# Kernel tuning notes

Measured on AMD Instinct MI355X. Metric: run time of the kernel, lower is better.

The kernel has to match this reference:

```python
import jax, jax.numpy as jnp
import numpy as np
from jax import lax

D_MODEL = 128

def _pad_same(x, kh, kw):
    ph, pw = kh - 1, kw - 1
    return jnp.pad(x, ((0, 0), (0, 0), (ph // 2, ph - ph // 2), (pw // 2, pw - pw // 2)))

def _conv(x, w, b):
    y = lax.conv_general_dilated(x, w, (1, 1), 'VALID', dimension_numbers=('NCHW', 'OIHW', 'NCHW'))
    return y + b[None, :, None, None]

def _group_norm(x, g, b, groups, eps=1e-5):
    N, C, H, W = x.shape
    xr = x.reshape(N, groups, -1)
    m = xr.mean(axis=2, keepdims=True)
    v = xr.var(axis=2, keepdims=True)
    xn = ((xr - m) / jnp.sqrt(v + eps)).reshape(N, C, H, W)
    return xn * g[None, :, None, None] + b[None, :, None, None]

def _maxpool(x, kh, kw):
    return lax.reduce_window(x, -jnp.inf, lax.max, (1, 1, kh, kw), (1, 1, kh, kw), 'VALID')

def _l2norm(x, axis):
    # torch F.normalize(p=2): x / max(||x||, eps)
    return x / jnp.maximum(jnp.linalg.norm(x, axis=axis, keepdims=True), 1e-12)

def _pos_encoding(S, d):
    pos = jnp.arange(S, dtype=jnp.float32)[:, None]
    div = jnp.exp(jnp.arange(0, d, 2, dtype=jnp.float32) * (-float(np.log(10000.0)) / d))
    pe = jnp.zeros((S, d), dtype=jnp.float32)
    pe = pe.at[:, 0::2].set(jnp.sin(pos * div)).at[:, 1::2].set(jnp.cos(pos * div))
    return pe

def setup_inputs() -> dict:
    key = jax.random.key(0)
    ks = jax.random.split(key, 16)
    def w(k, shape, fan_in):
        return jax.random.normal(k, shape, dtype=jnp.float32) * (1.0 / np.sqrt(fan_in))
    return {
        'x': jax.random.normal(ks[0], (1, 1024, 72, 64), dtype=jnp.float32),
        'conv1_w': w(ks[1], (32, 1, 6, 4), 1 * 6 * 4),
        'conv1_b': jnp.zeros((32,), jnp.float32),
        'gn1_g': jnp.ones((32,), jnp.float32), 'gn1_b': jnp.zeros((32,), jnp.float32),
        'conv2_w': w(ks[2], (64, 32, 6, 4), 32 * 6 * 4),
        'conv2_b': jnp.zeros((64,), jnp.float32),
        'gn2_g': jnp.ones((64,), jnp.float32), 'gn2_b': jnp.zeros((64,), jnp.float32),
        'conv3_w': w(ks[3], (128, 64, 6, 4), 64 * 6 * 4),
        'conv3_b': jnp.zeros((128,), jnp.float32),
        'gn3_g': jnp.ones((128,), jnp.float32), 'gn3_b': jnp.zeros((128,), jnp.float32),
        'fc1_w': w(ks[4], (128, 1024), 1024),
        'fc1_b': jnp.zeros((128,), jnp.float32),
        'wq': w(ks[5], (128, 128), 128), 'bq': jnp.zeros((128,), jnp.float32),
        'wk': w(ks[6], (128, 128), 128), 'bk': jnp.zeros((128,), jnp.float32),
        'wv': w(ks[7], (128, 128), 128), 'bv': jnp.zeros((128,), jnp.float32),
    }

def reference(x, conv1_w, conv1_b, gn1_g, gn1_b, conv2_w, conv2_b, gn2_g, gn2_b,
              conv3_w, conv3_b, gn3_g, gn3_b, fc1_w, fc1_b, wq, bq, wk, bk, wv, bv):
    selu = jax.nn.selu
    # x: [1, S, 72, 64] -> transpose(0,1): [S, 1, 72, 64] (S frames, 1 channel)
    h = jnp.transpose(x, (1, 0, 2, 3))
    h = _maxpool(_group_norm(selu(_conv(_pad_same(h, 6, 4), conv1_w, conv1_b)), gn1_g, gn1_b, 32), 2, 4)
    h = _maxpool(_group_norm(selu(_conv(_pad_same(h, 6, 4), conv2_w, conv2_b)), gn2_g, gn2_b, 32), 3, 4)
    h = _maxpool(_group_norm(selu(_conv(_pad_same(h, 6, 4), conv3_w, conv3_b)), gn3_g, gn3_b, 32), 3, 2)
    e = h.reshape(h.shape[0], -1)                       # [S, 1024]
    e = _l2norm(selu(e @ fc1_w.T + fc1_b), axis=1)      # [S, 128]
    S = e.shape[0]
    q = selu(e @ wq.T + bq)
    k = selu(e @ wk.T + bk)
    v = selu(e @ wv.T + bv)
    k_pos = k + _pos_encoding(S, D_MODEL)               # PE added to K only
    attn = jax.nn.softmax((q @ k_pos.T) / jnp.sqrt(jnp.float32(D_MODEL)), axis=-1)  # [S, S]
    # torch F.normalize default dim=1 on [1,S,D] -> normalize over the sequence axis
    out = _l2norm(attn @ v, axis=0) + e
    ea = _l2norm(out, axis=0)                           # [S, 128]
    # pairwise L2 distances (self-similarity matrix), then 1 - d/max(d)
    sq = jnp.sum(ea * ea, axis=1)
    d2 = jnp.maximum(sq[:, None] + sq[None, :] - 2.0 * (ea @ ea.T), 0.0)
    d = jnp.sqrt(d2 + 1e-12)
    return 1.0 - d / jnp.max(d)
```

## Files before the change

kernel.cpp:

```cpp
#include <hip/hip_runtime.h>
#include <hip/hip_bf16.h>
#include <math.h>

#define SELU_SCALE 1.0507009873554805f
#define SELU_SA    1.7580993408473766f

typedef __attribute__((ext_vector_type(8))) short short8;
typedef __attribute__((ext_vector_type(4))) short short4v;
typedef __attribute__((ext_vector_type(4))) float f32x4;

__device__ __forceinline__ float selu_f(float x){
    return x > 0.f ? SELU_SCALE * x : fmaf(SELU_SA, __expf(x), -SELU_SA);
}

__device__ __forceinline__ unsigned short bfc(float v){
    __hip_bfloat16 h = __float2bfloat16(v);
    return __builtin_bit_cast(unsigned short, h);
}
__device__ __forceinline__ float f_bf(unsigned short u){
    unsigned int x = ((unsigned int)u) << 16;
    return __builtin_bit_cast(float, x);
}

__device__ __forceinline__ float warp_max(float v){
    #pragma unroll
    for(int o=32;o>0;o>>=1) v = fmaxf(v,__shfl_down(v,o,64));
    return v;
}

__global__ void k_prep(const float* __restrict__ f1w, const float* __restrict__ wq,
                       const float* __restrict__ wk, const float* __restrict__ wv,
                       const float* __restrict__ w1, const float* __restrict__ w2,
                       const float* __restrict__ w3,
                       float* __restrict__ wt, float* __restrict__ wqt,
                       float* __restrict__ wkt, float* __restrict__ wvt,
                       short* __restrict__ w1bf, short* __restrict__ w2bf,
                       short* __restrict__ w3bf){
    int idx = blockIdx.x*256 + threadIdx.x;
    if(idx < 131072){ int r = idx >> 10, cc = idx & 1023; wt[cc*128 + r] = f1w[idx]; return; }
    idx -= 131072;
    if(idx < 16384){ int r = idx >> 7, cc = idx & 127; wqt[cc*128 + r] = wq[idx]; return; }
    idx -= 16384;
    if(idx < 16384){ int r = idx >> 7, cc = idx & 127; wkt[cc*128 + r] = wk[idx]; return; }
    idx -= 16384;
    if(idx < 16384){ int r = idx >> 7, cc = idx & 127; wvt[cc*128 + r] = wv[idx]; return; }
    idx -= 16384;
    if(idx < 49152){
        int t = idx >> 11, rem = idx & 2047;
        int oc = rem >> 5, ic = rem & 31;
        w2bf[idx] = (short)bfc(w2[oc*768 + ic*24 + t]);
        return;
    }
    idx -= 49152;
    if(idx < 196608){
        int t = idx >> 13, rem = idx & 8191;
        int oc = rem >> 6, ic = rem & 63;
        w3bf[idx] = (short)bfc(w3[oc*1536 + ic*24 + t]);
        return;
    }
    idx -= 196608;
    if(idx < 1024){
        int oc = idx >> 5, k = idx & 31;
        w1bf[idx] = (k < 24) ? (short)bfc(w1[oc*24 + k]) : (short)0;
    }
}

__global__ __launch_bounds__(768,1) void k_conv1m(
    const float* __restrict__ x, const short* __restrict__ w1bf,
    const float* __restrict__ bias, const float* __restrict__ g,
    const float* __restrict__ be, float* __restrict__ out)
{
    int s = blockIdx.x, tid = threadIdx.x;
    int l = tid & 63, wv = tid >> 6;
    int c = l & 15, qr = l >> 4;
    __shared__ char smem[127728];
    short* sdup = (short*)smem;
    char* pmaxb = smem + 41712;
    char* pminb = smem + 83184;
    float* sredf = (float*)(smem + 124656);
    __shared__ float scsh[64];

    const float* xs = x + (size_t)s*4608;
    for(int i = tid; i < 5056; i += 768){
        int yp = i >> 6, xx = i & 63;
        unsigned long long pk = 0ull;
        if(yp >= 2 && yp < 74){
            const float* row = xs + (yp-2)*64;
            #pragma unroll
            for(int t=0;t<4;t++){
                int cp = xx + t;
                float f = (cp>=1 && cp<65) ? row[cp-1] : 0.f;
                pk |= (unsigned long long)bfc(f) << (16*t);
            }
        }
        *(unsigned long long*)((char*)sdup + yp*528 + (xx&3)*128 + (xx>>2)*8) = pk;
    }
    short8 a0 = *(const short8*)(w1bf + c*32 + qr*8);
    short8 a1 = *(const short8*)(w1bf + (16+c)*32 + qr*8);
    float bias8[8];
    #pragma unroll
    for(int t=0;t<2;t++)
        #pragma unroll
        for(int r=0;r<4;r++) bias8[t*4+r] = bias[t*16 + qr*4 + r];
    float ssum8[8], ssq8[8];
    #pragma unroll
    for(int i=0;i<8;i++){ ssum8[i]=0.f; ssq8[i]=0.f; }
    __syncthreads();

    #pragma unroll 1
    for(int u=0; u<3; u++){
        int py = wv*3 + u;
        float pmx[8], pmn[8];
        #pragma unroll
        for(int i=0;i<8;i++){ pmx[i]=-INFINITY; pmn[i]=INFINITY; }
        #pragma unroll
        for(int off=0; off<4; off++){
            const char* bb = (const char*)sdup + off*128 + c*8;
            #pragma unroll
            for(int rr=0; rr<2; rr++){
                int y = py*2 + rr;
                short4v lo = *(const short4v*)(bb + (y+2*qr)*528);
                short4v hi = *(const short4v*)(bb + (y+2*qr+1)*528);
                short8 bfrag = __builtin_shufflevector(lo, hi, 0,1,2,3,4,5,6,7);
                f32x4 d0 = __builtin_amdgcn_mfma_f32_16x16x32_bf16(a0, bfrag, (f32x4){0.f,0.f,0.f,0.f}, 0,0,0);
                f32x4 d1 = __builtin_amdgcn_mfma_f32_16x16x32_bf16(a1, bfrag, (f32x4){0.f,0.f,0.f,0.f}, 0,0,0);
                #pragma unroll
                for(int r=0;r<4;r++){
                    float v0 = selu_f(d0[r] + bias8[r]);
                    float v1 = selu_f(d1[r] + bias8[4+r]);
                    ssum8[r]   += v0; ssq8[r]   = fmaf(v0,v0,ssq8[r]);
                    ssum8[4+r] += v1; ssq8[4+r] = fmaf(v1,v1,ssq8[4+r]);
                    pmx[r]   = fmaxf(pmx[r],   v0); pmn[r]   = fminf(pmn[r],   v0);
                    pmx[4+r] = fmaxf(pmx[4+r], v1); pmn[4+r] = fminf(pmn[4+r], v1);
                }
            }
        }
        int base = (py*16 + c)*72;
        #pragma unroll
        for(int t=0;t<2;t++){
            unsigned long long mpk=0ull, npk=0ull;
            #pragma unroll
            for(int r=0;r<4;r++){
                mpk |= (unsigned long long)bfc(pmx[t*4+r]) << (16*r);
                npk |= (unsigned long long)bfc(pmn[t*4+r]) << (16*r);
            }
            *(unsigned long long*)(pmaxb + base + t*32 + qr*8) = mpk;
            *(unsigned long long*)(pminb + base + t*32 + qr*8) = npk;
        }
    }
    #pragma unroll
    for(int off=1; off<16; off<<=1){
        #pragma unroll
        for(int i=0;i<8;i++){
            ssum8[i] += __shfl_xor(ssum8[i], off);
            ssq8[i]  += __shfl_xor(ssq8[i],  off);
        }
    }
    if(c == 0){
        #pragma unroll
        for(int i=0;i<8;i++){
            sredf[((wv*4 + qr)*8 + i)*2]     = ssum8[i];
            sredf[((wv*4 + qr)*8 + i)*2 + 1] = ssq8[i];
        }
    }
    __syncthreads();
    if(tid < 32){
        int oc = tid;
        int t = oc >> 4, rem = oc & 15, q = rem >> 2, r = rem & 3;
        int i = t*4 + r;
        float sum=0.f, sq=0.f;
        for(int w=0; w<12; w++){
            sum += sredf[((w*4+q)*8+i)*2];
            sq  += sredf[((w*4+q)*8+i)*2+1];
        }
        float mean = sum*(1.f/4608.f);
        float var  = sq*(1.f/4608.f) - mean*mean;
        float inv  = rsqrtf(var + 1e-5f);
        float sc = g[oc]*inv;
        scsh[oc*2]   = sc;
        scsh[oc*2+1] = be[oc] - mean*sc;
    }
    __syncthreads();
    float* ob = out + (size_t)s*18432;
    for(int i = tid; i < 18432; i += 768){
        int oc = i / 576, wpx = i - oc*576;
        float sc = scsh[oc*2], sh = scsh[oc*2+1];
        int boff = wpx*72 + oc*2;
        float vm = f_bf(*(unsigned short*)(pmaxb + boff));
        float vn = f_bf(*(unsigned short*)(pminb + boff));
        ob[i] = fmaf(sc, (sc >= 0.f) ? vm : vn, sh);
    }
}

__global__ __launch_bounds__(512,2) void k_conv2m(
    const float* __restrict__ in, const short* __restrict__ w2bf,
    const float* __restrict__ bias, const float* __restrict__ g,
    const float* __restrict__ be, float* __restrict__ out)
{
    int s = blockIdx.x, tid = threadIdx.x;
    int l = tid & 63, wv = tid >> 6;
    int ocp = wv >> 2, yq = wv & 3;
    int xc = l & 15, qr = l >> 4;
    __shared__ short sinb[26240];
    __shared__ float sred[2][4][2][4][2][2];
    int* zp = (int*)sinb;
    for(int i=tid;i<13120;i+=512) zp[i]=0;
    __syncthreads();
    const float* ibase = in + (size_t)s*18432;
    #pragma unroll
    for(int h=0;h<2;h++){
        int ic = (wv*2+h)*2;
        #pragma unroll
        for(int k=0;k<9;k++){
            int px = l + 64*k;
            float v0 = ibase[ic*576 + px];
            float v1 = ibase[(ic+1)*576 + px];
            int R = (px>>4)+2, C = (px&15)+1;
            int key = (C>>1)&3;
            int q0 = ic>>3;
            int byteoff = (R*20+C)*64 + (((q0^key)&3)<<4) + (ic&7)*2;
            *(unsigned int*)((char*)sinb + byteoff) =
                (unsigned int)bfc(v0) | ((unsigned int)bfc(v1)<<16);
        }
    }
    __syncthreads();
    f32x4 acc[2][9];
    #pragma unroll
    for(int o=0;o<2;o++)
        #pragma unroll
        for(int yt=0;yt<9;yt++) acc[o][yt] = (f32x4){0.f,0.f,0.f,0.f};
    const short8* wb = (const short8*)w2bf;
    int arow = ocp*32 + xc;
    short8 a0 = wb[arow*4 + qr];
    short8 a1 = wb[(arow+16)*4 + qr];
    char* sb = (char*)sinb;
    for(int tap=0; tap<24; tap++){
        short8 na0, na1;
        if(tap<23){
            na0 = wb[((tap+1)*64 + arow)*4 + qr];
            na1 = wb[((tap+1)*64 + arow + 16)*4 + qr];
        }
        int kh = tap>>2, kw = tap&3;
        int C = xc + kw;
        int cb = C*64 + (((qr ^ ((C>>1)&3))&3)<<4);
        int rb = (yq*9 + kh)*1280;
        #pragma unroll
        for(int yt=0;yt<9;yt++){
            short8 bf_ = *(const short8*)(sb + rb + yt*1280 + cb);
            acc[0][yt] = __builtin_amdgcn_mfma_f32_16x16x32_bf16(a0, bf_, acc[0][yt], 0,0,0);
            acc[1][yt] = __builtin_amdgcn_mfma_f32_16x16x32_bf16(a1, bf_, acc[1][yt], 0,0,0);
        }
        a0 = na0; a1 = na1;
    }
    #pragma unroll
    for(int o=0;o<2;o++){
        int ocb = (ocp*2+o)*16 + qr*4;
        float b0 = bias[ocb], b1 = bias[ocb+1], b2 = bias[ocb+2], b3 = bias[ocb+3];
        float s0=0,q0=0,s1=0,q1=0;
        #pragma unroll
        for(int yt=0;yt<9;yt++){
            float v0=selu_f(acc[o][yt][0]+b0), v1=selu_f(acc[o][yt][1]+b1);
            float v2=selu_f(acc[o][yt][2]+b2), v3=selu_f(acc[o][yt][3]+b3);
            acc[o][yt][0]=v0; acc[o][yt][1]=v1; acc[o][yt][2]=v2; acc[o][yt][3]=v3;
            s0+=v0+v1; q0+=v0*v0+v1*v1; s1+=v2+v3; q1+=v2*v2+v3*v3;
        }
        #pragma unroll
        for(int off=1;off<16;off<<=1){
            s0+=__shfl_xor(s0,off); q0+=__shfl_xor(q0,off);
            s1+=__shfl_xor(s1,off); q1+=__shfl_xor(q1,off);
        }
        if(xc==0){
            sred[ocp][yq][o][qr][0][0]=s0; sred[ocp][yq][o][qr][0][1]=q0;
            sred[ocp][yq][o][qr][1][0]=s1; sred[ocp][yq][o][qr][1][1]=q1;
        }
    }
    __syncthreads();
    float* ob = out + (size_t)s*64*48;
    #pragma unroll
    for(int o=0;o<2;o++){
        #pragma unroll
        for(int grp=0;grp<2;grp++){
            float ts=0, tq=0;
            #pragma unroll
            for(int y2=0;y2<4;y2++){ ts += sred[ocp][y2][o][qr][grp][0]; tq += sred[ocp][y2][o][qr][grp][1]; }
            float mean = ts*(1.f/1152.f);
            float var  = tq*(1.f/1152.f) - mean*mean;
            float inv  = rsqrtf(var + 1e-5f);
            int oc0 = (ocp*2+o)*16 + qr*4 + grp*2;
            float sc0 = g[oc0]*inv,   sh0 = be[oc0]   - mean*sc0;
            float sc1 = g[oc0+1]*inv, sh1 = be[oc0+1] - mean*sc1;
            #pragma unroll
            for(int yt=0;yt<9;yt++){
                acc[o][yt][grp*2]   = acc[o][yt][grp*2]*sc0 + sh0;
                acc[o][yt][grp*2+1] = acc[o][yt][grp*2+1]*sc1 + sh1;
            }
        }
        #pragma unroll
        for(int r=0;r<4;r++){
            #pragma unroll
            for(int py=0;py<3;py++){
                float m = fmaxf(fmaxf(acc[o][3*py][r],acc[o][3*py+1][r]),acc[o][3*py+2][r]);
                m = fmaxf(m, __shfl_xor(m,1));
                m = fmaxf(m, __shfl_xor(m,2));
                if((xc&3)==0){
                    int oc = (ocp*2+o)*16 + qr*4 + r;
                    ob[(size_t)oc*48 + (yq*3+py)*4 + (xc>>2)] = m;
                }
            }
        }
    }
}

__global__ __launch_bounds__(512,2) void k_conv3m(
    const float* __restrict__ in, const short* __restrict__ w3bf,
    const float* __restrict__ bias, const float* __restrict__ g,
    const float* __restrict__ be, float* __restrict__ e0)
{
    int sq = blockIdx.x, tid = threadIdx.x;
    int l = tid & 63, wv = tid >> 6;
    int ocp = wv >> 1, sL = wv & 1;
    int c = l & 15, qr = l >> 4;
    int yl = c >> 2, xl = c & 3;
    __shared__ char smem[49152];
    short* sinb = (short*)smem;
    int* zp = (int*)smem;
    for(int i=tid;i<8704;i+=512) zp[i]=0;
    __syncthreads();
    const float* ibase = in + (size_t)sq*6144;
    for(int j=0;j<6;j++){
        int idx = tid + 512*j;
        int px = idx % 48;
        int rest = idx / 48;
        int icp = rest & 31, ss = rest >> 5;
        int ic = icp*2;
        float v0 = ibase[ss*3072 + ic*48 + px];
        float v1 = ibase[ss*3072 + (ic+1)*48 + px];
        int R = (px>>2)+2, C = (px&3)+1;
        int pos = ss*136 + R*8 + C;
        int key = ((R&1)<<2) | (C&3);
        int q0 = ic>>3;
        int byteoff = pos*128 + (((q0^key)&7)<<4) + (ic&7)*2;
        *(unsigned int*)(smem + byteoff) = (unsigned int)bfc(v0) | ((unsigned int)bfc(v1)<<16);
    }
    __syncthreads();
    f32x4 acc[2][3];
    #pragma unroll
    for(int o=0;o<2;o++)
        #pragma unroll
        for(int yt=0;yt<3;yt++) acc[o][yt] = (f32x4){0.f,0.f,0.f,0.f};
    const short8* wb = (const short8*)w3bf;
    int arow = ocp*32 + c;
    char* sb = smem + sL*17408;
    short8 a0 = wb[arow*8 + qr];
    short8 a1 = wb[(arow+16)*8 + qr];
    for(int t2=0; t2<48; t2++){
        short8 na0, na1;
        if(t2<47){
            int nt = t2+1;
            na0 = wb[((nt>>1)*128 + arow)*8 + (nt&1)*4 + qr];
            na1 = wb[((nt>>1)*128 + arow + 16)*8 + (nt&1)*4 + qr];
        }
        int tap = t2>>1, ks = t2&1;
        int kh = tap>>2, kw = tap&3;
        int C = xl + kw;
        int q0 = ks*4 + qr;
        #pragma unroll
        for(int yt=0;yt<3;yt++){
            int R = yt*4 + yl + kh;
            int key = ((R&1)<<2) | (C&3);
            short8 bf_ = *(const short8*)(sb + (R*8+C)*128 + (((q0^key)&7)<<4));
            acc[0][yt] = __builtin_amdgcn_mfma_f32_16x16x32_bf16(a0, bf_, acc[0][yt], 0,0,0);
            acc[1][yt] = __builtin_amdgcn_mfma_f32_16x16x32_bf16(a1, bf_, acc[1][yt], 0,0,0);
        }
        a0 = na0; a1 = na1;
    }
    #pragma unroll
    for(int o=0;o<2;o++){
        int ocb = (ocp*2+o)*16 + qr*4;
        float b0 = bias[ocb], b1 = bias[ocb+1], b2 = bias[ocb+2], b3 = bias[ocb+3];
        float ssum=0.f, ssq=0.f;
        #pragma unroll
        for(int yt=0;yt<3;yt++){
            float v0=selu_f(acc[o][yt][0]+b0), v1=selu_f(acc[o][yt][1]+b1);
            float v2=selu_f(acc[o][yt][2]+b2), v3=selu_f(acc[o][yt][3]+b3);
            acc[o][yt][0]=v0; acc[o][yt][1]=v1; acc[o][yt][2]=v2; acc[o][yt][3]=v3;
            ssum += v0+v1+v2+v3; ssq += v0*v0+v1*v1+v2*v2+v3*v3;
        }
        #pragma unroll
        for(int off=1;off<16;off<<=1){ ssum+=__shfl_xor(ssum,off); ssq+=__shfl_xor(ssq,off); }
        float mean = ssum*(1.f/192.f);
        float var  = ssq*(1.f/192.f) - mean*mean;
        float inv  = rsqrtf(var + 1e-5f);
        #pragma unroll
        for(int r=0;r<4;r++){
            int oc = ocb + r;
            float sc = g[oc]*inv, sh = be[oc] - mean*sc;
            #pragma unroll
            for(int yt=0;yt<3;yt++) acc[o][yt][r] = acc[o][yt][r]*sc + sh;
        }
    }
    __syncthreads();
    float* scr = (float*)smem + wv*1536;
    #pragma unroll
    for(int o=0;o<2;o++)
        #pragma unroll
        for(int yt=0;yt<3;yt++)
            #pragma unroll
            for(int r=0;r<4;r++){
                int px = (yt*4+yl)*4 + xl;
                scr[o*768 + (qr*4+r)*48 + px] = acc[o][yt][r];
            }
    __syncthreads();
    float* sr = (float*)smem + wv*1536 + (l>>5)*768 + ((l>>1)&15)*48;
    int x2 = l&1;
    float* eo = e0 + (size_t)(sq*2+sL)*1024 + ((size_t)(ocp*2 + (l>>5))*16 + ((l>>1)&15))*8;
    #pragma unroll
    for(int py=0;py<4;py++){
        float m = sr[(py*3)*4 + x2*2];
        m = fmaxf(m, sr[(py*3)*4 + x2*2+1]);
        m = fmaxf(m, sr[(py*3+1)*4 + x2*2]);
        m = fmaxf(m, sr[(py*3+1)*4 + x2*2+1]);
        m = fmaxf(m, sr[(py*3+2)*4 + x2*2]);
        m = fmaxf(m, sr[(py*3+2)*4 + x2*2+1]);
        eo[py*2 + x2] = m;
    }
}

__global__ __launch_bounds__(512) void k_fcqkv(
    const float* __restrict__ e0, const float* __restrict__ wt,
    const float* __restrict__ bias, float* __restrict__ e,
    const float* __restrict__ wqt, const float* __restrict__ bq,
    const float* __restrict__ wkt, const float* __restrict__ bk,
    const float* __restrict__ wvt, const float* __restrict__ bv,
    float* __restrict__ q, float* __restrict__ kp, float* __restrict__ v)
{
    int s0 = blockIdx.x*4, tid = threadIdx.x;
    int j = tid & 127, q4 = tid >> 7;
    __shared__ float se[4][1024];
    __shared__ float sp[4][4][128];
    __shared__ float sredn[4][2];
    __shared__ float se2[4][128];
    __shared__ float sp3[3][4][4][128];
    for(int i=tid;i<4096;i+=512){
        int sl = i >> 10, ii = i & 1023;
        se[sl][ii] = e0[(size_t)(s0+sl)*1024 + ii];
    }
    __syncthreads();
    float acc[4] = {0.f,0.f,0.f,0.f};
    const float* wp = wt + (size_t)q4*256*128 + j;
    const int ibase = q4*256;
    #pragma unroll 4
    for(int i=0;i<256;i++){
        float w = wp[(size_t)i*128];
        #pragma unroll
        for(int sl=0;sl<4;sl++) acc[sl] = fmaf(se[sl][ibase+i], w, acc[sl]);
    }
    #pragma unroll
    for(int sl=0;sl<4;sl++) sp[sl][q4][j] = acc[sl];
    __syncthreads();
    int sl2 = q4, lane = tid & 63, wv_ = tid >> 6;
    float vfc = selu_f(bias[j] + sp[sl2][0][j] + sp[sl2][1][j] + sp[sl2][2][j] + sp[sl2][3][j]);
    float a = vfc*vfc;
    #pragma unroll
    for(int o=1;o<64;o<<=1) a += __shfl_xor(a, o);
    if(lane==0) sredn[sl2][wv_&1] = a;
    __syncthreads();
    float den = fmaxf(sqrtf(sredn[sl2][0]+sredn[sl2][1]), 1e-12f);
    float ev = vfc/den;
    se2[sl2][j] = ev;
    e[(size_t)(s0+sl2)*128 + j] = ev;
    __syncthreads();
    float aq[4]={0,0,0,0}, ak[4]={0,0,0,0}, av[4]={0,0,0,0};
    int i0b = q4*32;
    #pragma unroll 4
    for(int i=0;i<32;i++){
        float wqv = wqt[(i0b+i)*128 + j];
        float wkv = wkt[(i0b+i)*128 + j];
        float wvv = wvt[(i0b+i)*128 + j];
        #pragma unroll
        for(int sl=0;sl<4;sl++){
            float f = se2[sl][i0b+i];
            aq[sl] = fmaf(f, wqv, aq[sl]);
            ak[sl] = fmaf(f, wkv, ak[sl]);
            av[sl] = fmaf(f, wvv, av[sl]);
        }
    }
    #pragma unroll
    for(int sl=0;sl<4;sl++){
        sp3[0][sl][q4][j] = aq[sl];
        sp3[1][sl][q4][j] = ak[sl];
        sp3[2][sl][q4][j] = av[sl];
    }
    __syncthreads();
    float vq = selu_f(bq[j] + sp3[0][sl2][0][j]+sp3[0][sl2][1][j]+sp3[0][sl2][2][j]+sp3[0][sl2][3][j]);
    float vk = selu_f(bk[j] + sp3[1][sl2][0][j]+sp3[1][sl2][1][j]+sp3[1][sl2][2][j]+sp3[1][sl2][3][j]);
    float vv = selu_f(bv[j] + sp3[2][sl2][0][j]+sp3[2][sl2][1][j]+sp3[2][sl2][2][j]+sp3[2][sl2][3][j]);
    int i2 = j & ~1;
    float dv = __expf(-(float)i2 * 0.07195578412155481f);
    float ang = (float)(s0+sl2) * dv;
    float pe = (j & 1) ? cosf(ang) : sinf(ang);
    q[(size_t)(s0+sl2)*128+j]  = vq;
    kp[(size_t)(s0+sl2)*128+j] = vk + pe;
    v[(size_t)(s0+sl2)*128+j]  = vv;
}

__global__ __launch_bounds__(512) void k_attnav(
    const float* __restrict__ q, const float* __restrict__ kp,
    const float* __restrict__ v, float* __restrict__ av)
{
    int s0 = blockIdx.x*4, tid = threadIdx.x;
    __shared__ float4 sq4[4][32];
    __shared__ float p[4][1024];
    __shared__ float spart[4][4][128];
    __shared__ float smx[4][2], ssm[4][2];
    ((float*)sq4)[tid] = q[(size_t)s0*128 + tid];
    __syncthreads();
    #pragma unroll
    for(int h=0;h<2;h++){
        int t = tid + h*512;
        const float4* kr = (const float4*)(kp + (size_t)t*128);
        float d[4] = {0.f,0.f,0.f,0.f};
        #pragma unroll 4
        for(int i=0;i<32;i++){
            float4 kv = kr[i];
            #pragma unroll
            for(int sl=0;sl<4;sl++){
                float4 qv = sq4[sl][i];
                d[sl] += kv.x*qv.x + kv.y*qv.y + kv.z*qv.z + kv.w*qv.w;
            }
        }
        #pragma unroll
        for(int sl=0;sl<4;sl++) p[sl][t] = d[sl]*0.08838834764831845f;
    }
    __syncthreads();
    int sl2 = tid>>7, t2 = tid&127, lane = tid&63, wv_ = tid>>6;
    float vals[8];
    float m = -INFINITY;
    #pragma unroll
    for(int k=0;k<8;k++){ vals[k] = p[sl2][t2 + k*128]; m = fmaxf(m, vals[k]); }
    #pragma unroll
    for(int o=1;o<64;o<<=1) m = fmaxf(m, __shfl_xor(m,o));
    if(lane==0) smx[sl2][wv_&1] = m;
    __syncthreads();
    m = fmaxf(smx[sl2][0], smx[sl2][1]);
    float lsum = 0.f;
    #pragma unroll
    for(int k=0;k<8;k++){ vals[k] = __expf(vals[k]-m); lsum += vals[k]; }
    #pragma unroll
    for(int o=1;o<64;o<<=1) lsum += __shfl_xor(lsum,o);
    if(lane==0) ssm[sl2][wv_&1] = lsum;
    __syncthreads();
    float invs = 1.f/(ssm[sl2][0]+ssm[sl2][1]);
    #pragma unroll
    for(int k=0;k<8;k++) p[sl2][t2+k*128] = vals[k]*invs;
    __syncthreads();
    int j = tid & 127, q4 = tid >> 7;
    float acc[4] = {0,0,0,0};
    int t0 = q4*256;
    #pragma unroll 2
    for(int t=t0;t<t0+256;t++){
        float vv = v[(size_t)t*128 + j];
        #pragma unroll
        for(int sl=0;sl<4;sl++) acc[sl] = fmaf(p[sl][t], vv, acc[sl]);
    }
    #pragma unroll
    for(int sl=0;sl<4;sl++) spart[sl][q4][j] = acc[sl];
    __syncthreads();
    av[(size_t)(s0+sl2)*128 + j] = spart[sl2][0][j]+spart[sl2][1][j]+spart[sl2][2][j]+spart[sl2][3][j];
}

__global__ __launch_bounds__(1024) void k_colpipe(
    const float* __restrict__ av, const float* __restrict__ e, float* __restrict__ ea)
{
    int j = blockIdx.x, t = threadIdx.x;
    __shared__ float sred[16];
    int lane = t & 63, w = t >> 6;
    float vv = av[(size_t)t*128 + j];
    float ss = vv*vv;
    #pragma unroll
    for(int off=1;off<64;off<<=1) ss += __shfl_xor(ss,off);
    if(lane==0) sred[w]=ss;
    __syncthreads();
    float tot = 0.f;
    #pragma unroll
    for(int i=0;i<16;i++) tot += sred[i];
    float n1 = fmaxf(sqrtf(tot), 1e-12f);
    __syncthreads();
    float o = vv/n1 + e[(size_t)t*128 + j];
    float ss2 = o*o;
    #pragma unroll
    for(int off=1;off<64;off<<=1) ss2 += __shfl_xor(ss2,off);
    if(lane==0) sred[w]=ss2;
    __syncthreads();
    float tot2 = 0.f;
    #pragma unroll
    for(int i=0;i<16;i++) tot2 += sred[i];
    float n2 = fmaxf(sqrtf(tot2), 1e-12f);
    ea[(size_t)t*128 + j] = o/n2;
}

__global__ __launch_bounds__(256) void k_gram(
    const float* __restrict__ ea,
    float* __restrict__ d2, unsigned int* __restrict__ maxbits)
{
    int j0 = blockIdx.x*32, i0 = blockIdx.y*32, tid = threadIdx.x;
    __shared__ float sa[32*128];
    __shared__ float sb[32*128];
    __shared__ float sredm[32];
    __shared__ float sqa[32], sqb[32];
    for(int idx=tid;idx<4096;idx+=256){
        sa[idx] = ea[(size_t)i0*128 + idx];
        sb[idx] = ea[(size_t)j0*128 + idx];
    }
    __syncthreads();
    {
        int r = tid>>3, seg = tid&7;
        const float* A = sa + r*128 + seg*16;
        const float* B = sb + r*128 + seg*16;
        float pa=0.f, pb=0.f;
        #pragma unroll
        for(int i=0;i<16;i++){ pa = fmaf(A[i],A[i],pa); pb = fmaf(B[i],B[i],pb); }
        #pragma unroll
        for(int o=1;o<8;o<<=1){ pa += __shfl_xor(pa,o); pb += __shfl_xor(pb,o); }
        if(seg==0){ sqa[r]=pa; sqb[r]=pb; }
    }
    __syncthreads();
    float lm = 0.f;
    #pragma unroll
    for(int k2=0;k2<4;k2++){
        int pp = tid + k2*256;
        int li = pp>>5, lj = pp&31;
        const float4* A = (const float4*)(sa + li*128);
        const float4* B = (const float4*)(sb + lj*128);
        float acc=0.f;
        #pragma unroll 8
        for(int i=0;i<32;i++){
            float4 a=A[i], b=B[i];
            acc += a.x*b.x + a.y*b.y + a.z*b.z + a.w*b.w;
        }
        float dd = fmaxf(sqa[li] + sqb[lj] - 2.f*acc, 0.f);
        d2[(size_t)(i0+li)*1024 + j0+lj] = dd;
        lm = fmaxf(lm, dd);
    }
    lm = warp_max(lm);
    __syncthreads();
    if((tid&63)==0) sredm[tid>>6]=lm;
    __syncthreads();
    if(tid==0){
        float mm = fmaxf(fmaxf(sredm[0],sredm[1]),fmaxf(sredm[2],sredm[3]));
        atomicMax(maxbits, __float_as_uint(mm));
    }
}

__global__ __launch_bounds__(256) void k_final(
    const float* __restrict__ d2, const unsigned int* __restrict__ maxbits, float* __restrict__ out)
{
    int idx = blockIdx.x*256 + threadIdx.x;
    float md = sqrtf(__uint_as_float(*maxbits) + 1e-12f);
    out[idx] = 1.f - sqrtf(d2[idx] + 1e-12f)/md;
}

extern "C" void kernel_launch(void* const* d_in, const int* in_sizes, int n_in,
                              void* d_out, int out_size, void* d_ws, size_t ws_size,
                              hipStream_t stream)
{
    const float* x   = (const float*)d_in[0];
    const float* c1w = (const float*)d_in[1];  const float* c1b = (const float*)d_in[2];
    const float* g1g = (const float*)d_in[3];  const float* g1b = (const float*)d_in[4];
    const float* c2w = (const float*)d_in[5];  const float* c2b = (const float*)d_in[6];
    const float* g2g = (const float*)d_in[7];  const float* g2b = (const float*)d_in[8];
    const float* c3w = (const float*)d_in[9];  const float* c3b = (const float*)d_in[10];
    const float* g3g = (const float*)d_in[11]; const float* g3b = (const float*)d_in[12];
    const float* f1w = (const float*)d_in[13]; const float* f1b = (const float*)d_in[14];
    const float* wq  = (const float*)d_in[15]; const float* bq  = (const float*)d_in[16];
    const float* wk  = (const float*)d_in[17]; const float* bk  = (const float*)d_in[18];
    const float* wv  = (const float*)d_in[19]; const float* bv  = (const float*)d_in[20];

    float* W = (float*)d_ws;
    float* e0   = W;
    float* avb  = W + 2097152;
    float* eab  = W + 2228224;
    float* d2b  = W + 2359296;
    float* buf1 = W;
    float* buf2 = W + 18874368;
    float* wt   = W + 22020096;
    float* wqt  = W + 22151168;
    float* wkt  = W + 22167552;
    float* wvt  = W + 22183936;
    float* eb   = W + 22200320;
    float* qb   = W + 22331392;
    float* kpb  = W + 22462464;
    float* vb   = W + 22593536;
    unsigned int* maxb = (unsigned int*)(W + 22725632);
    short* w2bf = (short*)(W + 22725648);
    short* w3bf = (short*)(W + 22750224);
    short* w1bf = (short*)(W + 22848528);

    k_prep<<<1670,256,0,stream>>>(f1w, wq, wk, wv, c1w, c2w, c3w,
                                  wt, wqt, wkt, wvt, w1bf, w2bf, w3bf);

    k_conv1m<<<1024,768,0,stream>>>(x, w1bf, c1b, g1g, g1b, buf1);
    k_conv2m<<<1024,512,0,stream>>>(buf1, w2bf, c2b, g2g, g2b, buf2);
    k_conv3m<<<512,512,0,stream>>>(buf2, w3bf, c3b, g3g, g3b, e0);

    k_fcqkv<<<256,512,0,stream>>>(e0, wt, f1b, eb, wqt,bq, wkt,bk, wvt,bv, qb,kpb,vb);
    k_attnav<<<256,512,0,stream>>>(qb, kpb, vb, avb);

    hipMemsetAsync(maxb, 0, 4, stream);
    k_colpipe<<<128,1024,0,stream>>>(avb, eb, eab);
    k_gram<<<dim3(32,32),256,0,stream>>>(eab, d2b, maxb);
    k_final<<<4096,256,0,stream>>>(d2b, maxb, (float*)d_out);
}
```

Measured before the change: 367.9 us.

## Fuse conv2 and conv3 stages, store conv1 output as bf16, transpose e/av buffers

```diff
diff --git a/kernel.cpp b/kernel.cpp
--- a/kernel.cpp
+++ b/kernel.cpp
@@ -65,15 +65,15 @@
     }
 }
 
-__global__ __launch_bounds__(768,1) void k_conv1m(
+__global__ __launch_bounds__(1024,1) void k_conv1m(
     const float* __restrict__ x, const short* __restrict__ w1bf,
     const float* __restrict__ bias, const float* __restrict__ g,
-    const float* __restrict__ be, float* __restrict__ out)
+    const float* __restrict__ be, unsigned short* __restrict__ out)
 {
     int s = blockIdx.x, tid = threadIdx.x;
     int l = tid & 63, wv = tid >> 6;
     int c = l & 15, qr = l >> 4;
-    __shared__ char smem[127728];
+    __shared__ char smem[128752];
     short* sdup = (short*)smem;
     char* pmaxb = smem + 41712;
     char* pminb = smem + 83184;
@@ -81,7 +81,7 @@
     __shared__ float scsh[64];
 
     const float* xs = x + (size_t)s*4608;
-    for(int i = tid; i < 5056; i += 768){
+    for(int i = tid; i < 5056; i += 1024){
         int yp = i >> 6, xx = i & 63;
         unsigned long long pk = 0ull;
         if(yp >= 2 && yp < 74){
@@ -107,9 +107,11 @@
     for(int i=0;i<8;i++){ ssum8[i]=0.f; ssq8[i]=0.f; }
     __syncthreads();
 
+    int nu, py0;
+    if(wv < 4){ nu = 3; py0 = wv*3; } else { nu = 2; py0 = 12 + (wv-4)*2; }
     #pragma unroll 1
-    for(int u=0; u<3; u++){
-        int py = wv*3 + u;
+    for(int u=0; u<nu; u++){
+        int py = py0 + u;
         float pmx[8], pmn[8];
         #pragma unroll
         for(int i=0;i<8;i++){ pmx[i]=-INFINITY; pmn[i]=INFINITY; }
@@ -169,7 +171,7 @@
         int t = oc >> 4, rem = oc & 15, q = rem >> 2, r = rem & 3;
         int i = t*4 + r;
         float sum=0.f, sq=0.f;
-        for(int w=0; w<12; w++){
+        for(int w=0; w<16; w++){
             sum += sredf[((w*4+q)*8+i)*2];
             sq  += sredf[((w*4+q)*8+i)*2+1];
         }
@@ -181,46 +183,49 @@
         scsh[oc*2+1] = be[oc] - mean*sc;
     }
     __syncthreads();
-    float* ob = out + (size_t)s*18432;
-    for(int i = tid; i < 18432; i += 768){
+    unsigned short* ob = out + (size_t)s*18432;
+    for(int i = tid; i < 18432; i += 1024){
         int oc = i / 576, wpx = i - oc*576;
         float sc = scsh[oc*2], sh = scsh[oc*2+1];
         int boff = wpx*72 + oc*2;
         float vm = f_bf(*(unsigned short*)(pmaxb + boff));
         float vn = f_bf(*(unsigned short*)(pminb + boff));
-        ob[i] = fmaf(sc, (sc >= 0.f) ? vm : vn, sh);
-    }
-}
-
-__global__ __launch_bounds__(512,2) void k_conv2m(
-    const float* __restrict__ in, const short* __restrict__ w2bf,
-    const float* __restrict__ bias, const float* __restrict__ g,
-    const float* __restrict__ be, float* __restrict__ out)
+        ob[i] = bfc(fmaf(sc, (sc >= 0.f) ? vm : vn, sh));
+    }
+}
+
+__global__ __launch_bounds__(512,2) void k_conv23(
+    const unsigned short* __restrict__ in, const short* __restrict__ w2bf,
+    const float* __restrict__ b2, const float* __restrict__ g2,
+    const float* __restrict__ e2,
+    const short* __restrict__ w3bf,
+    const float* __restrict__ b3, const float* __restrict__ g3,
+    const float* __restrict__ e3, float* __restrict__ e0)
 {
     int s = blockIdx.x, tid = threadIdx.x;
     int l = tid & 63, wv = tid >> 6;
     int ocp = wv >> 2, yq = wv & 3;
     int xc = l & 15, qr = l >> 4;
-    __shared__ short sinb[26240];
-    __shared__ float sred[2][4][2][4][2][2];
-    int* zp = (int*)sinb;
-    for(int i=tid;i<13120;i+=512) zp[i]=0;
-    __syncthreads();
-    const float* ibase = in + (size_t)s*18432;
+    __shared__ char cs[69888];
+    short* sinb = (short*)cs;
+    char*  s3in = cs + 52480;
+    __shared__ float sredA[2][4][2][4][2][2];
+    for(int i=tid;i<17472;i+=512) ((int*)cs)[i] = 0;
+    __syncthreads();
+    const unsigned short* ibase = in + (size_t)s*18432;
     #pragma unroll
     for(int h=0;h<2;h++){
         int ic = (wv*2+h)*2;
         #pragma unroll
         for(int k=0;k<9;k++){
             int px = l + 64*k;
-            float v0 = ibase[ic*576 + px];
-            float v1 = ibase[(ic+1)*576 + px];
+            unsigned int v0 = ibase[ic*576 + px];
+            unsigned int v1 = ibase[(ic+1)*576 + px];
             int R = (px>>4)+2, C = (px&15)+1;
             int key = (C>>1)&3;
             int q0 = ic>>3;
             int byteoff = (R*20+C)*64 + (((q0^key)&3)<<4) + (ic&7)*2;
-            *(unsigned int*)((char*)sinb + byteoff) =
-                (unsigned int)bfc(v0) | ((unsigned int)bfc(v1)<<16);
+            *(unsigned int*)((char*)sinb + byteoff) = v0 | (v1<<16);
         }
     }
     __syncthreads();
@@ -255,40 +260,39 @@
     #pragma unroll
     for(int o=0;o<2;o++){
         int ocb = (ocp*2+o)*16 + qr*4;
-        float b0 = bias[ocb], b1 = bias[ocb+1], b2 = bias[ocb+2], b3 = bias[ocb+3];
-        float s0=0,q0=0,s1=0,q1=0;
+        float b0 = b2[ocb], b1 = b2[ocb+1], bb2 = b2[ocb+2], b3_ = b2[ocb+3];
+        float s0=0,q0s=0,s1=0,q1=0;
         #pragma unroll
         for(int yt=0;yt<9;yt++){
             float v0=selu_f(acc[o][yt][0]+b0), v1=selu_f(acc[o][yt][1]+b1);
-            float v2=selu_f(acc[o][yt][2]+b2), v3=selu_f(acc[o][yt][3]+b3);
+            float v2=selu_f(acc[o][yt][2]+bb2), v3=selu_f(acc[o][yt][3]+b3_);
             acc[o][yt][0]=v0; acc[o][yt][1]=v1; acc[o][yt][2]=v2; acc[o][yt][3]=v3;
-            s0+=v0+v1; q0+=v0*v0+v1*v1; s1+=v2+v3; q1+=v2*v2+v3*v3;
+            s0+=v0+v1; q0s+=v0*v0+v1*v1; s1+=v2+v3; q1+=v2*v2+v3*v3;
         }
         #pragma unroll
         for(int off=1;off<16;off<<=1){
-            s0+=__shfl_xor(s0,off); q0+=__shfl_xor(q0,off);
+            s0+=__shfl_xor(s0,off); q0s+=__shfl_xor(q0s,off);
             s1+=__shfl_xor(s1,off); q1+=__shfl_xor(q1,off);
         }
         if(xc==0){
-            sred[ocp][yq][o][qr][0][0]=s0; sred[ocp][yq][o][qr][0][1]=q0;
-            sred[ocp][yq][o][qr][1][0]=s1; sred[ocp][yq][o][qr][1][1]=q1;
-        }
-    }
-    __syncthreads();
-    float* ob = out + (size_t)s*64*48;
+            sredA[ocp][yq][o][qr][0][0]=s0; sredA[ocp][yq][o][qr][0][1]=q0s;
+            sredA[ocp][yq][o][qr][1][0]=s1; sredA[ocp][yq][o][qr][1][1]=q1;
+        }
+    }
+    __syncthreads();
     #pragma unroll
     for(int o=0;o<2;o++){
         #pragma unroll
         for(int grp=0;grp<2;grp++){
             float ts=0, tq=0;
             #pragma unroll
-            for(int y2=0;y2<4;y2++){ ts += sred[ocp][y2][o][qr][grp][0]; tq += sred[ocp][y2][o][qr][grp][1]; }
+            for(int y2=0;y2<4;y2++){ ts += sredA[ocp][y2][o][qr][grp][0]; tq += sredA[ocp][y2][o][qr][grp][1]; }
             float mean = ts*(1.f/1152.f);
             float var  = tq*(1.f/1152.f) - mean*mean;
             float inv  = rsqrtf(var + 1e-5f);
             int oc0 = (ocp*2+o)*16 + qr*4 + grp*2;
-            float sc0 = g[oc0]*inv,   sh0 = be[oc0]   - mean*sc0;
-            float sc1 = g[oc0+1]*inv, sh1 = be[oc0+1] - mean*sc1;
+            float sc0 = g2[oc0]*inv,   sh0 = e2[oc0]   - mean*sc0;
+            float sc1 = g2[oc0+1]*inv, sh1 = e2[oc0+1] - mean*sc1;
             #pragma unroll
             for(int yt=0;yt<9;yt++){
                 acc[o][yt][grp*2]   = acc[o][yt][grp*2]*sc0 + sh0;
@@ -304,61 +308,28 @@
                 m = fmaxf(m, __shfl_xor(m,2));
                 if((xc&3)==0){
                     int oc = (ocp*2+o)*16 + qr*4 + r;
-                    ob[(size_t)oc*48 + (yq*3+py)*4 + (xc>>2)] = m;
+                    int R = yq*3 + py + 2;
+                    int C = (xc>>2) + 1;
+                    int key = ((R&1)<<2) | (C&3);
+                    int q0 = oc>>3;
+                    *(unsigned short*)(s3in + (R*8+C)*128 + (((q0^key)&7)<<4) + (oc&7)*2) = bfc(m);
                 }
             }
         }
     }
-}
-
-__global__ __launch_bounds__(512,2) void k_conv3m(
-    const float* __restrict__ in, const short* __restrict__ w3bf,
-    const float* __restrict__ bias, const float* __restrict__ g,
-    const float* __restrict__ be, float* __restrict__ e0)
-{
-    int sq = blockIdx.x, tid = threadIdx.x;
-    int l = tid & 63, wv = tid >> 6;
-    int ocp = wv >> 1, sL = wv & 1;
-    int c = l & 15, qr = l >> 4;
-    int yl = c >> 2, xl = c & 3;
-    __shared__ char smem[49152];
-    short* sinb = (short*)smem;
-    int* zp = (int*)smem;
-    for(int i=tid;i<8704;i+=512) zp[i]=0;
-    __syncthreads();
-    const float* ibase = in + (size_t)sq*6144;
-    for(int j=0;j<6;j++){
-        int idx = tid + 512*j;
-        int px = idx % 48;
-        int rest = idx / 48;
-        int icp = rest & 31, ss = rest >> 5;
-        int ic = icp*2;
-        float v0 = ibase[ss*3072 + ic*48 + px];
-        float v1 = ibase[ss*3072 + (ic+1)*48 + px];
-        int R = (px>>2)+2, C = (px&3)+1;
-        int pos = ss*136 + R*8 + C;
-        int key = ((R&1)<<2) | (C&3);
-        int q0 = ic>>3;
-        int byteoff = pos*128 + (((q0^key)&7)<<4) + (ic&7)*2;
-        *(unsigned int*)(smem + byteoff) = (unsigned int)bfc(v0) | ((unsigned int)bfc(v1)<<16);
-    }
-    __syncthreads();
-    f32x4 acc[2][3];
-    #pragma unroll
-    for(int o=0;o<2;o++)
-        #pragma unroll
-        for(int yt=0;yt<3;yt++) acc[o][yt] = (f32x4){0.f,0.f,0.f,0.f};
-    const short8* wb = (const short8*)w3bf;
-    int arow = ocp*32 + c;
-    char* sb = smem + sL*17408;
-    short8 a0 = wb[arow*8 + qr];
-    short8 a1 = wb[(arow+16)*8 + qr];
+    __syncthreads();
+    int yl = xc >> 2, xl = xc & 3;
+    f32x4 acc3[3];
+    #pragma unroll
+    for(int yt=0;yt<3;yt++) acc3[yt] = (f32x4){0.f,0.f,0.f,0.f};
+    const short8* wb3 = (const short8*)w3bf;
+    int arow3 = wv*16 + xc;
+    short8 a3 = wb3[arow3*8 + qr];
     for(int t2=0; t2<48; t2++){
-        short8 na0, na1;
+        short8 na3;
         if(t2<47){
             int nt = t2+1;
-            na0 = wb[((nt>>1)*128 + arow)*8 + (nt&1)*4 + qr];
-            na1 = wb[((nt>>1)*128 + arow + 16)*8 + (nt&1)*4 + qr];
+            na3 = wb3[((nt>>1)*128 + arow3)*8 + (nt&1)*4 + qr];
         }
         int tap = t2>>1, ks = t2&1;
         int kh = tap>>2, kw = tap&3;
@@ -368,67 +339,53 @@
         for(int yt=0;yt<3;yt++){
             int R = yt*4 + yl + kh;
             int key = ((R&1)<<2) | (C&3);
-            short8 bf_ = *(const short8*)(sb + (R*8+C)*128 + (((q0^key)&7)<<4));
-            acc[0][yt] = __builtin_amdgcn_mfma_f32_16x16x32_bf16(a0, bf_, acc[0][yt], 0,0,0);
-            acc[1][yt] = __builtin_amdgcn_mfma_f32_16x16x32_bf16(a1, bf_, acc[1][yt], 0,0,0);
-        }
-        a0 = na0; a1 = na1;
-    }
-    #pragma unroll
-    for(int o=0;o<2;o++){
-        int ocb = (ocp*2+o)*16 + qr*4;
-        float b0 = bias[ocb], b1 = bias[ocb+1], b2 = bias[ocb+2], b3 = bias[ocb+3];
-        float ssum=0.f, ssq=0.f;
-        #pragma unroll
-        for(int yt=0;yt<3;yt++){
-            float v0=selu_f(acc[o][yt][0]+b0), v1=selu_f(acc[o][yt][1]+b1);
-            float v2=selu_f(acc[o][yt][2]+b2), v3=selu_f(acc[o][yt][3]+b3);
-            acc[o][yt][0]=v0; acc[o][yt][1]=v1; acc[o][yt][2]=v2; acc[o][yt][3]=v3;
-            ssum += v0+v1+v2+v3; ssq += v0*v0+v1*v1+v2*v2+v3*v3;
-        }
-        #pragma unroll
-        for(int off=1;off<16;off<<=1){ ssum+=__shfl_xor(ssum,off); ssq+=__shfl_xor(ssq,off); }
-        float mean = ssum*(1.f/192.f);
-        float var  = ssq*(1.f/192.f) - mean*mean;
-        float inv  = rsqrtf(var + 1e-5f);
-        #pragma unroll
-        for(int r=0;r<4;r++){
-            int oc = ocb + r;
-            float sc = g[oc]*inv, sh = be[oc] - mean*sc;
-            #pragma unroll
-            for(int yt=0;yt<3;yt++) acc[o][yt][r] = acc[o][yt][r]*sc + sh;
-        }
-    }
-    __syncthreads();
-    float* scr = (float*)smem + wv*1536;
-    #pragma unroll
-    for(int o=0;o<2;o++)
+            short8 bf_ = *(const short8*)(s3in + (R*8+C)*128 + (((q0^key)&7)<<4));
+            acc3[yt] = __builtin_amdgcn_mfma_f32_16x16x32_bf16(a3, bf_, acc3[yt], 0,0,0);
+        }
+        a3 = na3;
+    }
+    int ocb3 = wv*16 + qr*4;
+    float c0 = b3[ocb3], c1 = b3[ocb3+1], c2 = b3[ocb3+2], c3 = b3[ocb3+3];
+    float ssum=0.f, ssq=0.f;
+    #pragma unroll
+    for(int yt=0;yt<3;yt++){
+        float v0=selu_f(acc3[yt][0]+c0), v1=selu_f(acc3[yt][1]+c1);
+        float v2=selu_f(acc3[yt][2]+c2), v3=selu_f(acc3[yt][3]+c3);
+        acc3[yt][0]=v0; acc3[yt][1]=v1; acc3[yt][2]=v2; acc3[yt][3]=v3;
+        ssum += v0+v1+v2+v3; ssq += v0*v0+v1*v1+v2*v2+v3*v3;
+    }
+    #pragma unroll
+    for(int off=1;off<16;off<<=1){ ssum+=__shfl_xor(ssum,off); ssq+=__shfl_xor(ssq,off); }
+    float mean3 = ssum*(1.f/192.f);
+    float var3  = ssq*(1.f/192.f) - mean3*mean3;
+    float inv3  = rsqrtf(var3 + 1e-5f);
+    float* scr = (float*)cs + wv*768;
+    #pragma unroll
+    for(int r=0;r<4;r++){
+        int oc = ocb3 + r;
+        float sc = g3[oc]*inv3, sh = e3[oc] - mean3*sc;
         #pragma unroll
         for(int yt=0;yt<3;yt++)
-            #pragma unroll
-            for(int r=0;r<4;r++){
-                int px = (yt*4+yl)*4 + xl;
-                scr[o*768 + (qr*4+r)*48 + px] = acc[o][yt][r];
-            }
-    __syncthreads();
-    float* sr = (float*)smem + wv*1536 + (l>>5)*768 + ((l>>1)&15)*48;
-    int x2 = l&1;
-    float* eo = e0 + (size_t)(sq*2+sL)*1024 + ((size_t)(ocp*2 + (l>>5))*16 + ((l>>1)&15))*8;
-    #pragma unroll
-    for(int py=0;py<4;py++){
-        float m = sr[(py*3)*4 + x2*2];
-        m = fmaxf(m, sr[(py*3)*4 + x2*2+1]);
-        m = fmaxf(m, sr[(py*3+1)*4 + x2*2]);
-        m = fmaxf(m, sr[(py*3+1)*4 + x2*2+1]);
-        m = fmaxf(m, sr[(py*3+2)*4 + x2*2]);
-        m = fmaxf(m, sr[(py*3+2)*4 + x2*2+1]);
-        eo[py*2 + x2] = m;
+            scr[(qr*4+r)*48 + (yt*4+yl)*4 + xl] = acc3[yt][r]*sc + sh;
+    }
+    int oc_l = l>>2, pyw = l&3;
+    const float* srd = (const float*)cs + wv*768 + oc_l*48;
+    float* eo = e0 + (size_t)s*1024 + (wv*16 + oc_l)*8 + pyw*2;
+    #pragma unroll
+    for(int x2=0;x2<2;x2++){
+        float m = srd[(pyw*3)*4 + x2*2];
+        m = fmaxf(m, srd[(pyw*3)*4 + x2*2+1]);
+        m = fmaxf(m, srd[(pyw*3+1)*4 + x2*2]);
+        m = fmaxf(m, srd[(pyw*3+1)*4 + x2*2+1]);
+        m = fmaxf(m, srd[(pyw*3+2)*4 + x2*2]);
+        m = fmaxf(m, srd[(pyw*3+2)*4 + x2*2+1]);
+        eo[x2] = m;
     }
 }
 
 __global__ __launch_bounds__(512) void k_fcqkv(
     const float* __restrict__ e0, const float* __restrict__ wt,
-    const float* __restrict__ bias, float* __restrict__ e,
+    const float* __restrict__ bias, float* __restrict__ et,
     const float* __restrict__ wqt, const float* __restrict__ bq,
     const float* __restrict__ wkt, const float* __restrict__ bk,
     const float* __restrict__ wvt, const float* __restrict__ bv,
@@ -468,7 +425,7 @@
     float den = fmaxf(sqrtf(sredn[sl2][0]+sredn[sl2][1]), 1e-12f);
     float ev = vfc/den;
     se2[sl2][j] = ev;
-    e[(size_t)(s0+sl2)*128 + j] = ev;
+    et[(size_t)j*1024 + s0+sl2] = ev;
     __syncthreads();
     float aq[4]={0,0,0,0}, ak[4]={0,0,0,0}, av[4]={0,0,0,0};
     int i0b = q4*32;
@@ -506,7 +463,7 @@
 
 __global__ __launch_bounds__(512) void k_attnav(
     const float* __restrict__ q, const float* __restrict__ kp,
-    const float* __restrict__ v, float* __restrict__ av)
+    const float* __restrict__ v, float* __restrict__ avt)
 {
     int s0 = blockIdx.x*4, tid = threadIdx.x;
     __shared__ float4 sq4[4][32];
@@ -566,16 +523,16 @@
     #pragma unroll
     for(int sl=0;sl<4;sl++) spart[sl][q4][j] = acc[sl];
     __syncthreads();
-    av[(size_t)(s0+sl2)*128 + j] = spart[sl2][0][j]+spart[sl2][1][j]+spart[sl2][2][j]+spart[sl2][3][j];
+    avt[(size_t)j*1024 + s0+sl2] = spart[sl2][0][j]+spart[sl2][1][j]+spart[sl2][2][j]+spart[sl2][3][j];
 }
 
 __global__ __launch_bounds__(1024) void k_colpipe(
-    const float* __restrict__ av, const float* __restrict__ e, float* __restrict__ ea)
+    const float* __restrict__ avt, const float* __restrict__ et, float* __restrict__ ea)
 {
     int j = blockIdx.x, t = threadIdx.x;
     __shared__ float sred[16];
     int lane = t & 63, w = t >> 6;
-    float vv = av[(size_t)t*128 + j];
+    float vv = avt[(size_t)j*1024 + t];
     float ss = vv*vv;
     #pragma unroll
     for(int off=1;off<64;off<<=1) ss += __shfl_xor(ss,off);
@@ -586,7 +543,7 @@
     for(int i=0;i<16;i++) tot += sred[i];
     float n1 = fmaxf(sqrtf(tot), 1e-12f);
     __syncthreads();
-    float o = vv/n1 + e[(size_t)t*128 + j];
+    float o = vv/n1 + et[(size_t)j*1024 + t];
     float ss2 = o*o;
     #pragma unroll
     for(int off=1;off<64;off<<=1) ss2 += __shfl_xor(ss2,off);
@@ -678,36 +635,35 @@
 
     float* W = (float*)d_ws;
     float* e0   = W;
-    float* avb  = W + 2097152;
     float* eab  = W + 2228224;
     float* d2b  = W + 2359296;
-    float* buf1 = W;
-    float* buf2 = W + 18874368;
-    float* wt   = W + 22020096;
-    float* wqt  = W + 22151168;
-    float* wkt  = W + 22167552;
-    float* wvt  = W + 22183936;
-    float* eb   = W + 22200320;
-    float* qb   = W + 22331392;
-    float* kpb  = W + 22462464;
-    float* vb   = W + 22593536;
-    unsigned int* maxb = (unsigned int*)(W + 22725632);
-    short* w2bf = (short*)(W + 22725648);
-    short* w3bf = (short*)(W + 22750224);
-    short* w1bf = (short*)(W + 22848528);
+    unsigned short* buf1 = (unsigned short*)(W + 4194304);
+    float* wt   = W + 13631488;
+    float* wqt  = W + 13762560;
+    float* wkt  = W + 13778944;
+    float* wvt  = W + 13795328;
+    float* et   = W + 13811712;
+    float* qb   = W + 13942784;
+    float* kpb  = W + 14073856;
+    float* vb   = W + 14204928;
+    float* avt  = W + 14336000;
+    unsigned int* maxb = (unsigned int*)(W + 14467072);
+    short* w2bf = (short*)(W + 14467088);
+    short* w3bf = (short*)(W + 14491664);
+    short* w1bf = (short*)(W + 14589968);
 
     k_prep<<<1670,256,0,stream>>>(f1w, wq, wk, wv, c1w, c2w, c3w,
                                   wt, wqt, wkt, wvt, w1bf, w2bf, w3bf);
 
-    k_conv1m<<<1024,768,0,stream>>>(x, w1bf, c1b, g1g, g1b, buf1);
-    k_conv2m<<<1024,512,0,stream>>>(buf1, w2bf, c2b, g2g, g2b, buf2);
-    k_conv3m<<<512,512,0,stream>>>(buf2, w3bf, c3b, g3g, g3b, e0);
-
-    k_fcqkv<<<256,512,0,stream>>>(e0, wt, f1b, eb, wqt,bq, wkt,bk, wvt,bv, qb,kpb,vb);
-    k_attnav<<<256,512,0,stream>>>(qb, kpb, vb, avb);
+    k_conv1m<<<1024,1024,0,stream>>>(x, w1bf, c1b, g1g, g1b, buf1);
+    k_conv23<<<1024,512,0,stream>>>(buf1, w2bf, c2b, g2g, g2b,
+                                    w3bf, c3b, g3g, g3b, e0);
+
+    k_fcqkv<<<256,512,0,stream>>>(e0, wt, f1b, et, wqt,bq, wkt,bk, wvt,bv, qb,kpb,vb);
+    k_attnav<<<256,512,0,stream>>>(qb, kpb, vb, avt);
 
     hipMemsetAsync(maxb, 0, 4, stream);
-    k_colpipe<<<128,1024,0,stream>>>(avb, eb, eab);
+    k_colpipe<<<128,1024,0,stream>>>(avt, et, eab);
     k_gram<<<dim3(32,32),256,0,stream>>>(eab, d2b, maxb);
     k_final<<<4096,256,0,stream>>>(d2b, maxb, (float*)d_out);
 }
```

Result: faster. 360.2 us (median of 2 runs) (-2.1%).
